# Kernel optimization log

Measured on AMD Instinct MI355X. Metric: run time of the kernel, lower is better.

The kernel has to match this reference:

```python
import jax, jax.numpy as jnp
import numpy as np

NUM_AUDIOS = 64
NODES_PER = 800
N = NUM_AUDIOS * NODES_PER  # 51200
DEG = 8
E = N * DEG  # 409600
IN_C, HID, OUT, HEADS = 512, 256, 256, 2
NEG_SLOPE = 0.2  # PyG GATConv default


def setup_inputs() -> dict:
    key = jax.random.key(0)
    ks = jax.random.split(key, 12)
    x = jax.random.normal(ks[0], (N, IN_C), jnp.float32)
    # edges strictly inside each audio's node block (PyG batching: no cross-graph edges)
    src_l = jax.random.randint(ks[1], (NUM_AUDIOS, NODES_PER * DEG), 0, NODES_PER)
    dst_l = jax.random.randint(ks[2], (NUM_AUDIOS, NODES_PER * DEG), 0, NODES_PER)
    off = (jnp.arange(NUM_AUDIOS) * NODES_PER)[:, None]
    edge_index = jnp.stack([(src_l + off).reshape(-1), (dst_l + off).reshape(-1)]).astype(jnp.int32)
    batch = jnp.repeat(jnp.arange(NUM_AUDIOS), NODES_PER).astype(jnp.int32)

    def gl(k, shape, fan):
        return (jax.random.normal(k, shape, jnp.float32) / np.sqrt(fan)).astype(jnp.float32)

    W1 = gl(ks[3], (IN_C, HEADS * HID), IN_C)
    a_s1 = gl(ks[4], (HEADS, HID), HID)
    a_d1 = gl(ks[5], (HEADS, HID), HID)
    b1 = jnp.zeros((HID,), jnp.float32)
    W2 = gl(ks[6], (HID, HEADS * OUT), HID)
    a_s2 = gl(ks[7], (HEADS, OUT), OUT)
    a_d2 = gl(ks[8], (HEADS, OUT), OUT)
    b2 = jnp.zeros((OUT,), jnp.float32)
    w_att = gl(ks[9], (OUT, 1), OUT)
    b_att = jnp.zeros((1,), jnp.float32)
    w_cls = gl(ks[10], (OUT, 2), OUT)
    b_cls = jnp.zeros((2,), jnp.float32)
    return dict(x=x, edge_index=edge_index, batch=batch,
                W1=W1, a_s1=a_s1, a_d1=a_d1, b1=b1,
                W2=W2, a_s2=a_s2, a_d2=a_d2, b2=b2,
                w_att=w_att, b_att=b_att, w_cls=w_cls, b_cls=b_cls)


def _gat(x, src, dst, W, a_s, a_d, b):
    """PyG GATConv(heads=H, concat=False): linear -> per-edge LeakyReLU scores ->
    softmax over incoming edges (with self-loops) -> scatter-sum -> head-mean + bias."""
    n = x.shape[0]
    H, C = a_s.shape
    h = (x @ W).reshape(n, H, C)                      # [N,H,C]
    al_s = jnp.einsum('nhc,hc->nh', h, a_s)           # [N,H]
    al_d = jnp.einsum('nhc,hc->nh', h, a_d)
    loop = jnp.arange(n, dtype=src.dtype)             # add self-loops (default)
    s = jnp.concatenate([src, loop])
    d = jnp.concatenate([dst, loop])
    e = jax.nn.leaky_relu(al_s[s] + al_d[d], NEG_SLOPE)  # [E+N,H]
    mx = jax.ops.segment_max(e, d, num_segments=n)
    w = jnp.exp(e - mx[d])
    den = jax.ops.segment_sum(w, d, num_segments=n)
    alpha = w / den[d]
    out = jax.ops.segment_sum(h[s] * alpha[:, :, None], d, num_segments=n)  # [N,H,C]
    return out.mean(axis=1) + b


def reference(x, edge_index, batch, W1, a_s1, a_d1, b1, W2, a_s2, a_d2, b2,
              w_att, b_att, w_cls, b_cls):
    src, dst = edge_index[0], edge_index[1]
    h = jax.nn.relu(_gat(x, src, dst, W1, a_s1, a_d1, b1))
    node_emb = _gat(h, src, dst, W2, a_s2, a_d2, b2)
    # per-audio temporal attention: softmax over nodes within each audio segment.
    # (edges never cross audio boundaries, so the per-subgraph GAT re-run in the
    #  original Python loop equals the full-graph GAT restricted to each segment.)
    logits = node_emb @ w_att + b_att                 # [N,1]
    mx = jax.ops.segment_max(logits, batch, num_segments=NUM_AUDIOS)
    w = jnp.exp(logits - mx[batch])
    den = jax.ops.segment_sum(w, batch, num_segments=NUM_AUDIOS)
    attn = w / den[batch]                             # [N,1]
    attended = jax.ops.segment_sum(attn * node_emb, batch, num_segments=NUM_AUDIOS)  # [A,OUT]
    audio_result = attended @ w_cls + b_cls           # [A,2]
    return node_emb, audio_result
```

## Files before the change

kernel.cpp:

```cpp
#include <hip/hip_runtime.h>
#include <cstdint>
#include <cstddef>

#define NUM_AUDIOS 64
#define NODES_PER  800
#define NN         51200
#define EE         409600

typedef __attribute__((ext_vector_type(8))) unsigned short ushort8;
typedef __attribute__((ext_vector_type(4))) unsigned short ushort4v;
typedef __attribute__((ext_vector_type(8))) __bf16 bf16x8;
typedef __attribute__((ext_vector_type(4))) float f32x4;

__device__ __forceinline__ float b2f(unsigned short h) {
  return __uint_as_float(((unsigned)h) << 16);
}
__device__ __forceinline__ unsigned short f2b(float f) {
  unsigned u = __float_as_uint(f);
  u += 0x7fffu + ((u >> 16) & 1u);
  return (unsigned short)(u >> 16);
}
__device__ __forceinline__ float lrelu(float v) { return v > 0.f ? v : 0.2f * v; }

#define P_AS1 0
#define P_AD1 512
#define P_B1  1024
#define P_AS2 1536
#define P_AD2 2048
#define P_B2  2560
#define P_WATT 3072
#define P_BATT 3328
#define P_WCLS 3336
#define P_BCLS 3848

__global__ __launch_bounds__(256) void detect_k(const unsigned short* __restrict__ x,
                                                int* __restrict__ flag) {
  __shared__ int s;
  if (threadIdx.x == 0) s = 0;
  __syncthreads();
  int big = 0;
  for (int i = threadIdx.x; i < 4096; i += 256) {
    const float v = b2f(x[i]);
    if (!(__builtin_fabsf(v) <= 1e4f)) big = 1;
  }
  if (big) atomicOr(&s, 1);
  __syncthreads();
  if (threadIdx.x == 0) *flag = s;
}

__global__ __launch_bounds__(256) void conv_x_k(const void* __restrict__ xraw,
                                                unsigned short* __restrict__ x16,
                                                const int* __restrict__ flag) {
  const size_t i = ((size_t)blockIdx.x * 256 + threadIdx.x) * 4;
  if (*flag) {
    const float4 v = *(const float4*)((const float*)xraw + i);
    ushort4v o;
    o[0] = f2b(v.x); o[1] = f2b(v.y); o[2] = f2b(v.z); o[3] = f2b(v.w);
    *(ushort4v*)(x16 + i) = o;
  } else {
    *(ushort4v*)(x16 + i) = *(const ushort4v*)((const unsigned short*)xraw + i);
  }
}

__global__ __launch_bounds__(256) void conv_params_k(
    const void* p0, const void* p1, const void* p2, const void* p3, const void* p4,
    const void* p5, const void* p6, const void* p7, const void* p8, const void* p9,
    unsigned short* __restrict__ dst, const int* __restrict__ flag) {
  const void* srcs[10] = {p0, p1, p2, p3, p4, p5, p6, p7, p8, p9};
  const int offs[10] = {P_AS1, P_AD1, P_B1, P_AS2, P_AD2, P_B2, P_WATT, P_BATT, P_WCLS, P_BCLS};
  const int lens[10] = {512, 512, 256, 512, 512, 256, 256, 1, 512, 2};
  const int b = blockIdx.x;
  const int f = *flag;
  for (int i = threadIdx.x; i < lens[b]; i += 256) {
    dst[offs[b] + i] = f ? f2b(((const float*)srcs[b])[i])
                         : ((const unsigned short*)srcs[b])[i];
  }
}

__global__ __launch_bounds__(256) void transpose_k(const void* __restrict__ W,
                                                   unsigned short* __restrict__ WT,
                                                   const int* __restrict__ flag,
                                                   int K, int Nc) {
  const int idx = blockIdx.x * 256 + threadIdx.x;
  const int n = idx / K, k = idx - n * K;
  WT[idx] = (*flag) ? f2b(((const float*)W)[(size_t)k * Nc + n])
                    : ((const unsigned short*)W)[(size_t)k * Nc + n];
}

__global__ __launch_bounds__(256) void gemm_bt(const unsigned short* __restrict__ A,
                                               const unsigned short* __restrict__ BT,
                                               unsigned short* __restrict__ C,
                                               int K, int Nn) {
  __shared__ unsigned short As[128 * 32];
  __shared__ unsigned short Bs[128 * 32];
  const int tid = threadIdx.x;
  const int wave = tid >> 6, lane = tid & 63;
  const int m0 = blockIdx.y * 128, n0 = blockIdx.x * 128;
  const int wm = wave >> 1, wn = wave & 1;
  const int row = lane & 15, quad = lane >> 4;
  f32x4 acc[4][4];
#pragma unroll
  for (int i = 0; i < 4; ++i)
#pragma unroll
    for (int j = 0; j < 4; ++j) acc[i][j] = (f32x4){0.f, 0.f, 0.f, 0.f};

  for (int k0 = 0; k0 < K; k0 += 32) {
#pragma unroll
    for (int r = 0; r < 2; ++r) {
      const int cc = r * 256 + wave * 64 + lane;
      const int arow = cc >> 2, kc = (cc & 3) * 8;
      __builtin_amdgcn_global_load_lds(
          (const __attribute__((address_space(1))) void*)(A + (size_t)(m0 + arow) * K + k0 + kc),
          (__attribute__((address_space(3))) void*)(As + (size_t)(r * 256 + wave * 64) * 8),
          16, 0, 0);
      __builtin_amdgcn_global_load_lds(
          (const __attribute__((address_space(1))) void*)(BT + (size_t)(n0 + arow) * K + k0 + kc),
          (__attribute__((address_space(3))) void*)(Bs + (size_t)(r * 256 + wave * 64) * 8),
          16, 0, 0);
    }
    __syncthreads();

    bf16x8 af[4], bq[4];
#pragma unroll
    for (int i = 0; i < 4; ++i) {
      af[i] = *(const bf16x8*)&As[(wm * 64 + i * 16 + row) * 32 + quad * 8];
      bq[i] = *(const bf16x8*)&Bs[(wn * 64 + i * 16 + row) * 32 + quad * 8];
    }
#pragma unroll
    for (int i = 0; i < 4; ++i)
#pragma unroll
      for (int j = 0; j < 4; ++j)
        acc[i][j] = __builtin_amdgcn_mfma_f32_16x16x32_bf16(af[i], bq[j], acc[i][j], 0, 0, 0);
    __syncthreads();
  }

  const int col = lane & 15;
#pragma unroll
  for (int i = 0; i < 4; ++i)
#pragma unroll
    for (int j = 0; j < 4; ++j)
#pragma unroll
      for (int r = 0; r < 4; ++r) {
        const int gm = m0 + wm * 64 + i * 16 + quad * 4 + r;
        const int gn = n0 + wn * 64 + j * 16 + col;
        C[(size_t)gm * Nn + gn] = f2b(acc[i][j][r]);
      }
}

__global__ __launch_bounds__(256) void al_k(const unsigned short* __restrict__ h,
                                            const unsigned short* __restrict__ a_s,
                                            const unsigned short* __restrict__ a_d,
                                            float* __restrict__ al_s, float* __restrict__ al_d) {
  const int wave = threadIdx.x >> 6, lane = threadIdx.x & 63;
  const int n = blockIdx.x * 4 + wave;
  const ushort8 hv = *(const ushort8*)&h[(size_t)n * 512 + lane * 8];
  const ushort8 sv = *(const ushort8*)&a_s[lane * 8];
  const ushort8 dv = *(const ushort8*)&a_d[lane * 8];
  float ps = 0.f, pd = 0.f;
#pragma unroll
  for (int j = 0; j < 8; ++j) {
    const float hf = b2f(hv[j]);
    ps += hf * b2f(sv[j]);
    pd += hf * b2f(dv[j]);
  }
#pragma unroll
  for (int off = 1; off < 32; off <<= 1) {
    ps += __shfl_xor(ps, off);
    pd += __shfl_xor(pd, off);
  }
  if ((lane & 31) == 0) {
    const int head = lane >> 5;
    al_s[n * 2 + head] = ps;
    al_d[n * 2 + head] = pd;
  }
}

__global__ __launch_bounds__(256) void hist_k(const int* __restrict__ dst, int* __restrict__ counts) {
  const int e = blockIdx.x * 256 + threadIdx.x;
  atomicAdd(&counts[dst[e]], 1);
}

__global__ __launch_bounds__(256) void rowptr_k(const int* __restrict__ counts, int* __restrict__ row_ptr) {
  __shared__ int sh[800];
  __shared__ int pre[200];
  const int a = blockIdx.x, t = threadIdx.x;
  for (int i = t; i < 800; i += 256) sh[i] = counts[a * 800 + i];
  __syncthreads();
  if (t < 200) pre[t] = sh[t * 4] + sh[t * 4 + 1] + sh[t * 4 + 2] + sh[t * 4 + 3];
  __syncthreads();
  if (t == 0) {
    int run = 0;
    for (int i = 0; i < 200; ++i) { const int v = pre[i]; pre[i] = run; run += v; }
  }
  __syncthreads();
  if (t < 200) {
    int b = a * 6400 + pre[t];
#pragma unroll
    for (int j = 0; j < 4; ++j) { row_ptr[a * 800 + t * 4 + j] = b; b += sh[t * 4 + j]; }
  }
}

__global__ __launch_bounds__(256) void scatter_k(const int* __restrict__ src, const int* __restrict__ dst,
                                                 const int* __restrict__ row_ptr, int* __restrict__ cursor,
                                                 int* __restrict__ ssrc) {
  const int e = blockIdx.x * 256 + threadIdx.x;
  const int d = dst[e];
  const int p = atomicAdd(&cursor[d], 1);
  ssrc[row_ptr[d] + p] = src[e];
}

__global__ __launch_bounds__(256) void agg_k(const unsigned short* __restrict__ h,
                                             const float* __restrict__ al_s, const float* __restrict__ al_d,
                                             const int* __restrict__ row_ptr, const int* __restrict__ counts,
                                             const int* __restrict__ ssrc, const unsigned short* __restrict__ bias,
                                             unsigned short* __restrict__ out, int do_relu,
                                             void* __restrict__ out2, const int* __restrict__ flagp) {
  const int wave = threadIdx.x >> 6, lane = threadIdx.x & 63;
  const int b = blockIdx.x;
  const int g = b & 7, r = b >> 3;
  const int a = g + 8 * (r / 200);
  const int chunk = r % 200;
  const int n = a * 800 + chunk * 4 + wave;
  const int head = lane >> 5;
  const int deg = counts[n];
  const int base = row_ptr[n];
  const float ald = al_d[n * 2 + head];
  const float self_e = lrelu(al_s[n * 2 + head] + ald);
  float mx = self_e;
  for (int i = 0; i < deg; ++i) {
    const int s = ssrc[base + i];
    mx = fmaxf(mx, lrelu(al_s[s * 2 + head] + ald));
  }
  float acc[8];
  float den;
  {
    const float w = __expf(self_e - mx);
    den = w;
    const ushort8 hv = *(const ushort8*)&h[(size_t)n * 512 + lane * 8];
#pragma unroll
    for (int j = 0; j < 8; ++j) acc[j] = w * b2f(hv[j]);
  }
  for (int i = 0; i < deg; ++i) {
    const int s = ssrc[base + i];
    const float w = __expf(lrelu(al_s[s * 2 + head] + ald) - mx);
    den += w;
    const ushort8 hv = *(const ushort8*)&h[(size_t)s * 512 + lane * 8];
#pragma unroll
    for (int j = 0; j < 8; ++j) acc[j] += w * b2f(hv[j]);
  }
  const float inv = 1.f / den;
  const int c0 = (lane & 31) * 8;
  ushort8 res;
  float ov[8];
#pragma unroll
  for (int j = 0; j < 8; ++j) {
    const float mine = acc[j] * inv;
    const float other = __shfl_xor(mine, 32);
    float o = (mine + other) * 0.5f + b2f(bias[c0 + j]);
    if (do_relu) o = fmaxf(o, 0.f);
    ov[j] = o;
    res[j] = f2b(o);
  }
  if (lane < 32) {
    *(ushort8*)&out[(size_t)n * 256 + c0] = res;
    if (out2) {
      if (*flagp) {
        float4* p = (float4*)((float*)out2 + (size_t)n * 256 + c0);
        p[0] = (float4){ov[0], ov[1], ov[2], ov[3]};
        p[1] = (float4){ov[4], ov[5], ov[6], ov[7]};
      } else {
        *(ushort8*)((unsigned short*)out2 + (size_t)n * 256 + c0) = res;
      }
    }
  }
}

__global__ __launch_bounds__(256) void logits_k(const unsigned short* __restrict__ emb,
                                                const unsigned short* __restrict__ params,
                                                float* __restrict__ lg) {
  const int tid = threadIdx.x;
  const int half = tid >> 5, tc = tid & 31;
  const int n = blockIdx.x * 8 + half;
  const ushort8 ev = *(const ushort8*)&emb[(size_t)n * 256 + tc * 8];
  const ushort8 wv = *(const ushort8*)&params[P_WATT + tc * 8];
  float d = 0.f;
#pragma unroll
  for (int j = 0; j < 8; ++j) d += b2f(ev[j]) * b2f(wv[j]);
#pragma unroll
  for (int off = 1; off < 32; off <<= 1) d += __shfl_xor(d, off);
  if (tc == 0) lg[n] = d + b2f(params[P_BATT]);
}

__global__ __launch_bounds__(256) void stats_k(const float* __restrict__ lg,
                                               float* __restrict__ mxv, float* __restrict__ invv) {
  __shared__ float red[256];
  const int a = blockIdx.x, t = threadIdx.x;
  float m = -1e30f;
  for (int i = t; i < 800; i += 256) m = fmaxf(m, lg[a * 800 + i]);
  red[t] = m; __syncthreads();
  for (int s = 128; s >= 1; s >>= 1) { if (t < s) red[t] = fmaxf(red[t], red[t + s]); __syncthreads(); }
  const float mx = red[0];
  __syncthreads();
  float sum = 0.f;
  for (int i = t; i < 800; i += 256) sum += __expf(lg[a * 800 + i] - mx);
  red[t] = sum; __syncthreads();
  for (int s = 128; s >= 1; s >>= 1) { if (t < s) red[t] += red[t + s]; __syncthreads(); }
  if (t == 0) { mxv[a] = mx; invv[a] = 1.f / red[0]; }
}

__global__ __launch_bounds__(256) void attended_k(const unsigned short* __restrict__ emb,
                                                  const float* __restrict__ lg,
                                                  const float* __restrict__ mxv,
                                                  const float* __restrict__ invv,
                                                  float* __restrict__ attended) {
  const int b = blockIdx.x;
  const int a = b >> 3, chunk = b & 7;
  const int t = threadIdx.x;
  __shared__ float ws[100];
  const int i0 = chunk * 100;
  const float mx = mxv[a], inv = invv[a];
  if (t < 100) ws[t] = __expf(lg[a * 800 + i0 + t] - mx) * inv;
  __syncthreads();
  float acc = 0.f;
  const unsigned short* base = emb + ((size_t)(a * 800 + i0)) * 256 + t;
#pragma unroll 4
  for (int j = 0; j < 100; ++j) acc += ws[j] * b2f(base[(size_t)j * 256]);
  atomicAdd(&attended[a * 256 + t], acc);
}

__global__ __launch_bounds__(256) void cls_k(const float* __restrict__ attended,
                                             const unsigned short* __restrict__ params,
                                             void* __restrict__ out, const int* __restrict__ flag) {
  __shared__ float red[256];
  const int a = blockIdx.x, t = threadIdx.x;
  const float v = attended[a * 256 + t];
  const float p0 = v * b2f(params[P_WCLS + t * 2]);
  const float p1 = v * b2f(params[P_WCLS + t * 2 + 1]);
  red[t] = p0; __syncthreads();
  for (int s = 128; s >= 1; s >>= 1) { if (t < s) red[t] += red[t + s]; __syncthreads(); }
  const float r0 = red[0];
  __syncthreads();
  red[t] = p1; __syncthreads();
  for (int s = 128; s >= 1; s >>= 1) { if (t < s) red[t] += red[t + s]; __syncthreads(); }
  const float r1 = red[0];
  if (t == 0) {
    const float o0 = r0 + b2f(params[P_BCLS]);
    const float o1 = r1 + b2f(params[P_BCLS + 1]);
    if (*flag) {
      ((float*)out)[(size_t)NN * 256 + a * 2]     = o0;
      ((float*)out)[(size_t)NN * 256 + a * 2 + 1] = o1;
    } else {
      ((unsigned short*)out)[(size_t)NN * 256 + a * 2]     = f2b(o0);
      ((unsigned short*)out)[(size_t)NN * 256 + a * 2 + 1] = f2b(o1);
    }
  }
}

extern "C" void kernel_launch(void* const* d_in, const int* in_sizes, int n_in,
                              void* d_out, int out_size, void* d_ws, size_t ws_size,
                              hipStream_t stream) {
  (void)in_sizes; (void)n_in; (void)out_size; (void)ws_size;
  const void* x_raw  = d_in[0];
  const int*  eidx   = (const int*)d_in[1];
  const int* src = eidx;
  const int* dst = eidx + EE;

  char* ws = (char*)d_ws;
  size_t off = 0;
  auto alloc = [&](size_t bytes) -> void* {
    void* p = ws + off;
    off += (bytes + 255) & ~(size_t)255;
    return p;
  };
  int* flag              = (int*)alloc(256);
  unsigned short* params = (unsigned short*)alloc(4096 * 2);
  unsigned short* W1T    = (unsigned short*)alloc((size_t)512 * 512 * 2);
  unsigned short* W2T    = (unsigned short*)alloc((size_t)512 * 256 * 2);
  unsigned short* x16    = (unsigned short*)alloc((size_t)NN * 512 * 2);
  unsigned short* hbig   = (unsigned short*)alloc((size_t)NN * 512 * 2);
  float* al_s   = (float*)alloc((size_t)NN * 2 * 4);
  float* al_d   = (float*)alloc((size_t)NN * 2 * 4);
  int*   counts = (int*)alloc((size_t)NN * 4);
  int*   rowp   = (int*)alloc((size_t)NN * 4);
  int*   cursor = (int*)alloc((size_t)NN * 4);
  int*   ssrc   = (int*)alloc((size_t)EE * 4);
  float* lg     = (float*)alloc((size_t)NN * 4);
  float* mxv    = (float*)alloc(NUM_AUDIOS * 4);
  float* invv   = (float*)alloc(NUM_AUDIOS * 4);
  float* attended = (float*)alloc((size_t)NUM_AUDIOS * 256 * 4);
  unsigned short* hrel  = x16;
  unsigned short* emb16 = x16 + (size_t)NN * 256;

  detect_k<<<dim3(1), 256, 0, stream>>>((const unsigned short*)x_raw, flag);

  hipMemsetAsync(counts, 0, (size_t)NN * 4, stream);
  hipMemsetAsync(cursor, 0, (size_t)NN * 4, stream);
  hipMemsetAsync(attended, 0, (size_t)NUM_AUDIOS * 256 * 4, stream);

  conv_x_k<<<dim3(NN * 512 / 4 / 256), 256, 0, stream>>>(x_raw, x16, flag);
  conv_params_k<<<dim3(10), 256, 0, stream>>>(d_in[4], d_in[5], d_in[6], d_in[8], d_in[9],
                                              d_in[10], d_in[11], d_in[12], d_in[13], d_in[14],
                                              params, flag);
  transpose_k<<<dim3(512 * 512 / 256), 256, 0, stream>>>(d_in[3], W1T, flag, 512, 512);
  transpose_k<<<dim3(512 * 256 / 256), 256, 0, stream>>>(d_in[7], W2T, flag, 256, 512);

  hist_k<<<dim3(EE / 256), 256, 0, stream>>>(dst, counts);
  rowptr_k<<<dim3(NUM_AUDIOS), 256, 0, stream>>>(counts, rowp);
  scatter_k<<<dim3(EE / 256), 256, 0, stream>>>(src, dst, rowp, cursor, ssrc);

  gemm_bt<<<dim3(4, 400), 256, 0, stream>>>(x16, W1T, hbig, 512, 512);
  al_k<<<dim3(NN / 4), 256, 0, stream>>>(hbig, params + P_AS1, params + P_AD1, al_s, al_d);
  agg_k<<<dim3(NN / 4), 256, 0, stream>>>(hbig, al_s, al_d, rowp, counts, ssrc,
                                          params + P_B1, hrel, 1, nullptr, flag);

  gemm_bt<<<dim3(4, 400), 256, 0, stream>>>(hrel, W2T, hbig, 256, 512);
  al_k<<<dim3(NN / 4), 256, 0, stream>>>(hbig, params + P_AS2, params + P_AD2, al_s, al_d);
  agg_k<<<dim3(NN / 4), 256, 0, stream>>>(hbig, al_s, al_d, rowp, counts, ssrc,
                                          params + P_B2, emb16, 0, d_out, flag);

  logits_k<<<dim3(NN / 8), 256, 0, stream>>>(emb16, params, lg);
  stats_k<<<dim3(NUM_AUDIOS), 256, 0, stream>>>(lg, mxv, invv);
  attended_k<<<dim3(NUM_AUDIOS * 8), 256, 0, stream>>>(emb16, lg, mxv, invv, attended);
  cls_k<<<dim3(NUM_AUDIOS), 256, 0, stream>>>(attended, params, d_out, flag);
}
```

Before: 492.3 us.

## Parallelize edge softmax across lanes in aggregation and fuse logits into agg

The aggregation kernel now has the lanes of each half-wave load neighbour indices and attention scores in parallel. It computes the max from the raw source scores, using the fact that LeakyReLU is monotonic, and broadcasts the weights and indices with shuffles before the feature gather. This replaces two serial per-edge loops that re-read the index and score arrays. The per-node attention logit is also computed inside the second aggregation, so the separate logits kernel and its re-read of the embeddings are removed. Address arithmetic moves to 32-bit unsigned, which adds an overflow assumption on the index sizes.

```diff
diff --git a/kernel.cpp b/kernel.cpp
--- a/kernel.cpp
+++ b/kernel.cpp
@@ -214,7 +214,9 @@
                                              const int* __restrict__ row_ptr, const int* __restrict__ counts,
                                              const int* __restrict__ ssrc, const unsigned short* __restrict__ bias,
                                              unsigned short* __restrict__ out, int do_relu,
-                                             void* __restrict__ out2, const int* __restrict__ flagp) {
+                                             void* __restrict__ out2, const int* __restrict__ flagp,
+                                             const unsigned short* __restrict__ watt,
+                                             float* __restrict__ lg) {
   const int wave = threadIdx.x >> 6, lane = threadIdx.x & 63;
   const int b = blockIdx.x;
   const int g = b & 7, r = b >> 3;
@@ -222,34 +224,51 @@
   const int chunk = r % 200;
   const int n = a * 800 + chunk * 4 + wave;
   const int head = lane >> 5;
+  const int hl = lane & 31;
+  const int hsel = lane & 32;
   const int deg = counts[n];
   const int base = row_ptr[n];
   const float ald = al_d[n * 2 + head];
   const float self_e = lrelu(al_s[n * 2 + head] + ald);
-  float mx = self_e;
-  for (int i = 0; i < deg; ++i) {
+
+  float m = -1e30f;
+  for (int i = hl; i < deg; i += 32) {
     const int s = ssrc[base + i];
-    mx = fmaxf(mx, lrelu(al_s[s * 2 + head] + ald));
-  }
+    m = fmaxf(m, al_s[s * 2 + head]);
+  }
+#pragma unroll
+  for (int off = 1; off < 32; off <<= 1) m = fmaxf(m, __shfl_xor(m, off));
+  const float mx = fmaxf(lrelu(m + ald), self_e);
+
+  const float w_self = __expf(self_e - mx);
   float acc[8];
-  float den;
   {
-    const float w = __expf(self_e - mx);
-    den = w;
-    const ushort8 hv = *(const ushort8*)&h[(size_t)n * 512 + lane * 8];
-#pragma unroll
-    for (int j = 0; j < 8; ++j) acc[j] = w * b2f(hv[j]);
-  }
-  for (int i = 0; i < deg; ++i) {
-    const int s = ssrc[base + i];
-    const float w = __expf(lrelu(al_s[s * 2 + head] + ald) - mx);
-    den += w;
-    const ushort8 hv = *(const ushort8*)&h[(size_t)s * 512 + lane * 8];
-#pragma unroll
-    for (int j = 0; j < 8; ++j) acc[j] += w * b2f(hv[j]);
-  }
-  const float inv = 1.f / den;
-  const int c0 = (lane & 31) * 8;
+    const ushort8 hv = *(const ushort8*)&h[(unsigned)(n * 512 + lane * 8)];
+#pragma unroll
+    for (int j = 0; j < 8; ++j) acc[j] = w_self * b2f(hv[j]);
+  }
+  float dpart = 0.f;
+  for (int t0 = 0; t0 < deg; t0 += 32) {
+    const int cnt = min(32, deg - t0);
+    int s = 0; float w = 0.f;
+    if (hl < cnt) {
+      s = ssrc[base + t0 + hl];
+      w = __expf(lrelu(al_s[s * 2 + head] + ald) - mx);
+      dpart += w;
+    }
+    for (int i = 0; i < cnt; ++i) {
+      const float wb = __shfl(w, hsel + i);
+      const int sb = __shfl(s, hsel + i);
+      const ushort8 hv = *(const ushort8*)&h[(unsigned)(sb * 512 + lane * 8)];
+#pragma unroll
+      for (int j = 0; j < 8; ++j) acc[j] += wb * b2f(hv[j]);
+    }
+  }
+#pragma unroll
+  for (int off = 1; off < 32; off <<= 1) dpart += __shfl_xor(dpart, off);
+  const float inv = 1.f / (w_self + dpart);
+
+  const int c0 = hl * 8;
   ushort8 res;
   float ov[8];
 #pragma unroll
@@ -262,7 +281,7 @@
     res[j] = f2b(o);
   }
   if (lane < 32) {
-    *(ushort8*)&out[(size_t)n * 256 + c0] = res;
+    *(ushort8*)&out[(unsigned)(n * 256 + c0)] = res;
     if (out2) {
       if (*flagp) {
         float4* p = (float4*)((float*)out2 + (size_t)n * 256 + c0);
@@ -272,23 +291,16 @@
         *(ushort8*)((unsigned short*)out2 + (size_t)n * 256 + c0) = res;
       }
     }
-  }
-}
-
-__global__ __launch_bounds__(256) void logits_k(const unsigned short* __restrict__ emb,
-                                                const unsigned short* __restrict__ params,
-                                                float* __restrict__ lg) {
-  const int tid = threadIdx.x;
-  const int half = tid >> 5, tc = tid & 31;
-  const int n = blockIdx.x * 8 + half;
-  const ushort8 ev = *(const ushort8*)&emb[(size_t)n * 256 + tc * 8];
-  const ushort8 wv = *(const ushort8*)&params[P_WATT + tc * 8];
-  float d = 0.f;
-#pragma unroll
-  for (int j = 0; j < 8; ++j) d += b2f(ev[j]) * b2f(wv[j]);
-#pragma unroll
-  for (int off = 1; off < 32; off <<= 1) d += __shfl_xor(d, off);
-  if (tc == 0) lg[n] = d + b2f(params[P_BATT]);
+    if (lg) {
+      const ushort8 wv = *(const ushort8*)&watt[c0];
+      float d = 0.f;
+#pragma unroll
+      for (int j = 0; j < 8; ++j) d += ov[j] * b2f(wv[j]);
+#pragma unroll
+      for (int off = 1; off < 32; off <<= 1) d += __shfl_xor(d, off);
+      if (hl == 0) lg[n] = d + b2f(watt[256]);
+    }
+  }
 }
 
 __global__ __launch_bounds__(256) void stats_k(const float* __restrict__ lg,
@@ -411,14 +423,15 @@
   gemm_bt<<<dim3(4, 400), 256, 0, stream>>>(x16, W1T, hbig, 512, 512);
   al_k<<<dim3(NN / 4), 256, 0, stream>>>(hbig, params + P_AS1, params + P_AD1, al_s, al_d);
   agg_k<<<dim3(NN / 4), 256, 0, stream>>>(hbig, al_s, al_d, rowp, counts, ssrc,
-                                          params + P_B1, hrel, 1, nullptr, flag);
+                                          params + P_B1, hrel, 1, nullptr, flag,
+                                          params + P_WATT, nullptr);
 
   gemm_bt<<<dim3(4, 400), 256, 0, stream>>>(hrel, W2T, hbig, 256, 512);
   al_k<<<dim3(NN / 4), 256, 0, stream>>>(hbig, params + P_AS2, params + P_AD2, al_s, al_d);
   agg_k<<<dim3(NN / 4), 256, 0, stream>>>(hbig, al_s, al_d, rowp, counts, ssrc,
-                                          params + P_B2, emb16, 0, d_out, flag);
-
-  logits_k<<<dim3(NN / 8), 256, 0, stream>>>(emb16, params, lg);
+                                          params + P_B2, emb16, 0, d_out, flag,
+                                          params + P_WATT, lg);
+
   stats_k<<<dim3(NUM_AUDIOS), 256, 0, stream>>>(lg, mxv, invv);
   attended_k<<<dim3(NUM_AUDIOS * 8), 256, 0, stream>>>(emb16, lg, mxv, invv, attended);
   cls_k<<<dim3(NUM_AUDIOS), 256, 0, stream>>>(attended, params, d_out, flag);
```

Result: faster. 448.0 us (-9.0%).
